# Optimization experiments

Measured on AMD Instinct MI355X. Metric: run time of the kernel, lower is better.

Reference implementation:

```python
import jax, jax.numpy as jnp
import numpy as np

HIDDEN = 4096
NUM_HEADS = 32
HEAD_DIM = HIDDEN // NUM_HEADS


def _fp8_roundtrip(x):
    # emulate torch float8_e4m3fn weight storage
    return x.astype(jnp.float8_e4m3fn).astype(jnp.float32)


def setup_inputs() -> dict:
    key = jax.random.key(0)
    ks = jax.random.split(key, 10)
    B, S = 2, 4096
    hidden_states = jax.random.normal(ks[0], (B, S, HIDDEN), dtype=jnp.float32)
    scale = 0.02
    def lin(kw, kb):
        w = jax.random.normal(kw, (HIDDEN, HIDDEN), dtype=jnp.float32) * scale
        b = jax.random.normal(kb, (HIDDEN,), dtype=jnp.float32) * scale
        return w, b
    wq, bq = lin(ks[1], ks[2])
    wk, bk = lin(ks[3], ks[4])
    wv, bv = lin(ks[5], ks[6])
    wl, bl = lin(ks[7], ks[8])
    # fp8-quantized Q/K/V projections (latent projection stays fp32)
    wq, bq = _fp8_roundtrip(wq), _fp8_roundtrip(bq)
    wk, bk = _fp8_roundtrip(wk), _fp8_roundtrip(bk)
    wv, bv = _fp8_roundtrip(wv), _fp8_roundtrip(bv)
    return {"hidden_states": hidden_states, "wq": wq, "bq": bq, "wk": wk,
            "bk": bk, "wv": wv, "bv": bv, "wl": wl, "bl": bl}


def reference(hidden_states, wq, bq, wk, bk, wv, bv, wl, bl):
    B, S, E = hidden_states.shape
    H, D = NUM_HEADS, HEAD_DIM
    q = (hidden_states @ wq.T + bq).reshape(B, S, H, D)
    k = (hidden_states @ wk.T + bk).reshape(B, S, H, D)
    v = (hidden_states @ wv.T + bv).reshape(B, S, H, D)
    latent = hidden_states @ wl.T + bl  # computed but unused, as in source
    # NOTE: source does NOT transpose to [B,H,S,D]; scores are [B,S,H,H]
    scores = jnp.einsum('bshd,bstd->bsht', q, k) / np.sqrt(D).astype(np.float32)
    probs = jax.nn.softmax(scores, axis=-1)
    context = jnp.einsum('bsht,bstd->bshd', probs, v).reshape(B, S, E)
    return context
```

## Files before the change

### kernel.cpp

```cpp
#include <hip/hip_runtime.h>
#include <stdint.h>

#define HIDDEN 4096
#define M_TOK 8192
#define KDIM 4096

typedef __attribute__((ext_vector_type(8))) __bf16 bf16x8;
typedef __attribute__((ext_vector_type(4))) float f32x4;
typedef __attribute__((ext_vector_type(8))) unsigned short u16x8;

#define GAS __attribute__((address_space(1)))
#define LAS __attribute__((address_space(3)))

__device__ __forceinline__ unsigned short f2bf(float f) {
  unsigned int u = __float_as_uint(f);
  u += 0x7FFFu + ((u >> 16) & 1u);
  return (unsigned short)(u >> 16);
}
__device__ __forceinline__ float bf2f(unsigned short b) {
  return __uint_as_float(((unsigned int)b) << 16);
}

__device__ __forceinline__ void cvt8(const float* __restrict__ in,
                                     unsigned short* __restrict__ out, int i) {
  const f32x4* p = (const f32x4*)in + (size_t)2 * i;
  f32x4 a = p[0], b = p[1];
  u16x8 o;
  o[0] = f2bf(a.x); o[1] = f2bf(a.y); o[2] = f2bf(a.z); o[3] = f2bf(a.w);
  o[4] = f2bf(b.x); o[5] = f2bf(b.y); o[6] = f2bf(b.z); o[7] = f2bf(b.w);
  ((u16x8*)out)[i] = o;
}

__global__ __launch_bounds__(256) void cvt_fused(
    const float* __restrict__ hs, const float* __restrict__ wq,
    const float* __restrict__ wk, const float* __restrict__ wv,
    const float* __restrict__ bq, const float* __restrict__ bk,
    const float* __restrict__ bv,
    unsigned short* __restrict__ hsb, unsigned short* __restrict__ wb,
    float* __restrict__ bias) {
  int b = blockIdx.x;
  int tid = threadIdx.x;
  if (b < 16384) {
    cvt8(hs, hsb, b * 256 + tid);
  } else if (b < 24576) {
    cvt8(wq, wb, (b - 16384) * 256 + tid);
  } else if (b < 32768) {
    cvt8(wk, wb + 16777216, (b - 24576) * 256 + tid);
  } else if (b < 40960) {
    cvt8(wv, wb + 33554432, (b - 32768) * 256 + tid);
  } else {
    int i = (b - 40960) * 256 + tid;
    float v = (i < 4096) ? bq[i] : (i < 8192) ? bk[i - 4096] : bv[i - 8192];
    bias[i] = v;
  }
}

#define BAR() __builtin_amdgcn_s_barrier()
#define PRIO(p) __builtin_amdgcn_s_setprio(p)
#define VMC6() asm volatile("s_waitcnt vmcnt(6)" ::: "memory")
#define VMC0() asm volatile("s_waitcnt vmcnt(0)" ::: "memory")
#define LGKM0() do { asm volatile("s_waitcnt lgkmcnt(0)" ::: "memory"); \
  __builtin_amdgcn_sched_barrier(0); } while (0)
#define SB0() __builtin_amdgcn_sched_barrier(0)

__global__ __launch_bounds__(512, 2) void gemm_qkv(
    const unsigned short* __restrict__ A,
    const unsigned short* __restrict__ W,
    const float* __restrict__ bias,
    unsigned short* __restrict__ out) {
  __shared__ __attribute__((aligned(16))) unsigned short lds[65536];

  int tid = threadIdx.x;
  int lane = tid & 63;
  int w = tid >> 6;
  int wm = w >> 2;
  int wn = w & 3;
  int l16 = lane & 15;
  int lk = lane >> 4;

  int bid = blockIdx.x;
  int xcd = bid & 7;
  int local = bid >> 3;
  int r = local >> 5;
  int i = local & 31;
  int tm = (xcd << 2) + (i >> 3);
  int tn = (r << 3) + (i & 7);
  int m0 = tm << 8, n0 = tn << 8;

  int rp = tid >> 3;
  int ce = ((tid & 7) << 3) ^ ((rp & 7) << 3);
  const unsigned short* aSrc = A + (size_t)(m0 + rp) * KDIM + ce;
  const unsigned short* bSrc = W + (size_t)(n0 + rp) * KDIM + ce;
  int tid8 = tid * 8;

#define STA(b, h, kt) do { \
  __builtin_amdgcn_global_load_lds((GAS void*)(aSrc + (size_t)((h)*128) * KDIM + (kt)*64), \
      (LAS void*)(lds + (b)*16384 + (h)*8192 + tid8), 16, 0, 0); \
  __builtin_amdgcn_global_load_lds((GAS void*)(aSrc + (size_t)((h)*128 + 64) * KDIM + (kt)*64), \
      (LAS void*)(lds + (b)*16384 + (h)*8192 + 4096 + tid8), 16, 0, 0); } while (0)
#define STB(b, h, kt) do { \
  __builtin_amdgcn_global_load_lds((GAS void*)(bSrc + (size_t)((h)*128) * KDIM + (kt)*64), \
      (LAS void*)(lds + 32768 + (b)*16384 + (h)*8192 + tid8), 16, 0, 0); \
  __builtin_amdgcn_global_load_lds((GAS void*)(bSrc + (size_t)((h)*128 + 64) * KDIM + (kt)*64), \
      (LAS void*)(lds + 32768 + (b)*16384 + (h)*8192 + 4096 + tid8), 16, 0, 0); } while (0)

  int colbase = (lk << 3) ^ ((l16 & 7) << 3);
  int aRd = wm * 8192 + l16 * 64 + colbase;
  int bRd = (wn >> 1) * 8192 + (wn & 1) * 4096 + l16 * 64 + colbase;

#define RD_A(c, mi, ks) (*(const bf16x8*)(lds + (c)*16384 + (((aRd) + (mi)*1024) ^ ((ks)*32))))
#define RD_B(c, nj, ks) (*(const bf16x8*)(lds + 32768 + (c)*16384 + (((bRd) + (nj)*1024) ^ ((ks)*32))))

  bf16x8 av[8][2];
  bf16x8 bv[4][2];
  f32x4 acc[8][4] = {};

#define RP1(c) do { \
  bv[0][0]=RD_B(c,0,0); bv[0][1]=RD_B(c,0,1); bv[1][0]=RD_B(c,1,0); bv[1][1]=RD_B(c,1,1); \
  bv[2][0]=RD_B(c,2,0); bv[2][1]=RD_B(c,2,1); bv[3][0]=RD_B(c,3,0); bv[3][1]=RD_B(c,3,1); \
  av[0][0]=RD_A(c,0,0); av[0][1]=RD_A(c,0,1); av[1][0]=RD_A(c,1,0); av[1][1]=RD_A(c,1,1); } while (0)
#define RP2(c) do { \
  av[2][0]=RD_A(c,2,0); av[2][1]=RD_A(c,2,1); av[3][0]=RD_A(c,3,0); av[3][1]=RD_A(c,3,1); \
  av[4][0]=RD_A(c,4,0); av[4][1]=RD_A(c,4,1); av[5][0]=RD_A(c,5,0); av[5][1]=RD_A(c,5,1); } while (0)
#define RP3(c) do { \
  av[6][0]=RD_A(c,6,0); av[6][1]=RD_A(c,6,1); av[7][0]=RD_A(c,7,0); av[7][1]=RD_A(c,7,1); } while (0)

#define MFMA2(mi, nj) do { \
  acc[mi][nj] = __builtin_amdgcn_mfma_f32_16x16x32_bf16(av[mi][0], bv[nj][0], acc[mi][nj], 0, 0, 0); \
  acc[mi][nj] = __builtin_amdgcn_mfma_f32_16x16x32_bf16(av[mi][1], bv[nj][1], acc[mi][nj], 0, 0, 0); } while (0)
#define MM(mi) do { MFMA2(mi,0); MFMA2(mi,1); MFMA2(mi,2); MFMA2(mi,3); } while (0)

#define KTILE(c, ka, kb) do { \
  STA(!(c), 1, ka); \
  BAR(); LGKM0(); PRIO(1); MM(0); MM(1); RP2(c); PRIO(0); SB0(); BAR(); \
  STB(c, 0, kb); \
  BAR(); LGKM0(); PRIO(1); MM(2); MM(3); RP3(c); PRIO(0); SB0(); BAR(); \
  STB(c, 1, kb); \
  BAR(); LGKM0(); PRIO(1); MM(4); MM(5); PRIO(0); SB0(); BAR(); \
  STA(c, 0, kb); VMC6(); \
  BAR(); SB0(); PRIO(1); MM(6); MM(7); RP1(!(c)); PRIO(0); SB0(); BAR(); } while (0)

  STB(0, 0, 0); STB(0, 1, 0); STA(0, 0, 0); STA(0, 1, 0);
  STB(1, 0, 1); STB(1, 1, 1); STA(1, 0, 1);
  VMC0();
  BAR();
  RP1(0);

  for (int it = 0; it < 31; ++it) {
    int k1 = 2 * it + 1, k2 = 2 * it + 2, k3 = 2 * it + 3;
    KTILE(0, k1, k2);
    KTILE(1, k2, k3);
  }
  STA(1, 1, 63);
  BAR(); LGKM0(); PRIO(1); MM(0); MM(1); RP2(0); PRIO(0); SB0(); BAR();
  BAR(); LGKM0(); PRIO(1); MM(2); MM(3); RP3(0); PRIO(0); SB0(); BAR();
  BAR(); LGKM0(); PRIO(1); MM(4); MM(5); PRIO(0); SB0(); BAR();
  VMC0();
  BAR(); SB0(); PRIO(1); MM(6); MM(7); RP1(1); PRIO(0); SB0(); BAR();
  BAR(); LGKM0(); PRIO(1); MM(0); MM(1); RP2(1); PRIO(0); SB0(); BAR();
  BAR(); LGKM0(); PRIO(1); MM(2); MM(3); RP3(1); PRIO(0); SB0(); BAR();
  BAR(); LGKM0(); PRIO(1); MM(4); MM(5); PRIO(0); SB0(); BAR();
  BAR(); LGKM0(); PRIO(1); MM(6); MM(7); PRIO(0);

  int matc = n0 >> 12;
  int ncol = (n0 & 4095) + wn * 64;
  unsigned short* O = out + (size_t)matc * M_TOK * HIDDEN;
  float bb[4];
#pragma unroll
  for (int nj = 0; nj < 4; ++nj) bb[nj] = bias[n0 + wn * 64 + nj * 16 + l16];
#pragma unroll
  for (int mi = 0; mi < 8; ++mi) {
#pragma unroll
    for (int rr = 0; rr < 4; ++rr) {
      int row = m0 + wm * 128 + mi * 16 + lk * 4 + rr;
      size_t rb = (size_t)row * HIDDEN + ncol + l16;
#pragma unroll
      for (int nj = 0; nj < 4; ++nj)
        O[rb + nj * 16] = f2bf(acc[mi][nj][rr] + bb[nj]);
    }
  }
}

__global__ __launch_bounds__(256) void attn_kernel(const unsigned short* __restrict__ qkv,
                                                   float* __restrict__ out) {
  __shared__ float sQ[32 * 132];
  __shared__ float sK[32 * 132];
  __shared__ float sV[32 * 132];
  __shared__ float sP[32 * 33];

  int m = blockIdx.x;
  int tid = threadIdx.x;
  const unsigned short* gq = qkv + (size_t)m * HIDDEN;
  const unsigned short* gk = gq + (size_t)M_TOK * HIDDEN;
  const unsigned short* gv = gk + (size_t)M_TOK * HIDDEN;

  int row = tid >> 3;
  int cb = (tid & 7) << 4;
  int go = row * 128 + cb;
  int lo = row * 132 + cb;
  {
    u16x8 x0 = *(const u16x8*)(gq + go);
    u16x8 x1 = *(const u16x8*)(gq + go + 8);
#pragma unroll
    for (int j = 0; j < 8; ++j) { sQ[lo + j] = bf2f(x0[j]); sQ[lo + 8 + j] = bf2f(x1[j]); }
    x0 = *(const u16x8*)(gk + go);
    x1 = *(const u16x8*)(gk + go + 8);
#pragma unroll
    for (int j = 0; j < 8; ++j) { sK[lo + j] = bf2f(x0[j]); sK[lo + 8 + j] = bf2f(x1[j]); }
    x0 = *(const u16x8*)(gv + go);
    x1 = *(const u16x8*)(gv + go + 8);
#pragma unroll
    for (int j = 0; j < 8; ++j) { sV[lo + j] = bf2f(x0[j]); sV[lo + 8 + j] = bf2f(x1[j]); }
  }
  __syncthreads();

  int h = tid >> 3;
  int t4 = (tid & 7) << 2;
  const f32x4* qr = (const f32x4*)(sQ + h * 132);
  const f32x4* k0 = (const f32x4*)(sK + (t4 + 0) * 132);
  const f32x4* k1 = (const f32x4*)(sK + (t4 + 1) * 132);
  const f32x4* k2 = (const f32x4*)(sK + (t4 + 2) * 132);
  const f32x4* k3 = (const f32x4*)(sK + (t4 + 3) * 132);
  float s0 = 0.f, s1 = 0.f, s2 = 0.f, s3 = 0.f;
#pragma unroll
  for (int d = 0; d < 32; ++d) {
    f32x4 q = qr[d];
    f32x4 a = k0[d]; s0 += q.x * a.x + q.y * a.y + q.z * a.z + q.w * a.w;
    f32x4 b = k1[d]; s1 += q.x * b.x + q.y * b.y + q.z * b.z + q.w * b.w;
    f32x4 c = k2[d]; s2 += q.x * c.x + q.y * c.y + q.z * c.z + q.w * c.w;
    f32x4 e = k3[d]; s3 += q.x * e.x + q.y * e.y + q.z * e.z + q.w * e.w;
  }
  const float scale = 0.08838834764831845f;
  s0 *= scale; s1 *= scale; s2 *= scale; s3 *= scale;
  float mx = fmaxf(fmaxf(s0, s1), fmaxf(s2, s3));
  mx = fmaxf(mx, __shfl_xor(mx, 1));
  mx = fmaxf(mx, __shfl_xor(mx, 2));
  mx = fmaxf(mx, __shfl_xor(mx, 4));
  float e0 = __expf(s0 - mx), e1 = __expf(s1 - mx), e2 = __expf(s2 - mx), e3 = __expf(s3 - mx);
  float sum = e0 + e1 + e2 + e3;
  sum += __shfl_xor(sum, 1);
  sum += __shfl_xor(sum, 2);
  sum += __shfl_xor(sum, 4);
  float inv = 1.0f / sum;
  sP[h * 33 + t4 + 0] = e0 * inv;
  sP[h * 33 + t4 + 1] = e1 * inv;
  sP[h * 33 + t4 + 2] = e2 * inv;
  sP[h * 33 + t4 + 3] = e3 * inv;
  __syncthreads();

  int d0 = (tid & 7) << 4;
  f32x4 o0 = {0.f, 0.f, 0.f, 0.f}, o1 = o0, o2 = o0, o3 = o0;
  const float* pr = sP + h * 33;
#pragma unroll
  for (int t = 0; t < 32; ++t) {
    float p = pr[t];
    const f32x4* vr = (const f32x4*)(sV + t * 132 + d0);
    o0 += p * vr[0];
    o1 += p * vr[1];
    o2 += p * vr[2];
    o3 += p * vr[3];
  }
  f32x4* op = (f32x4*)(out + (size_t)m * HIDDEN + h * 128 + d0);
  op[0] = o0; op[1] = o1; op[2] = o2; op[3] = o3;
}

extern "C" void kernel_launch(void* const* d_in, const int* in_sizes, int n_in,
                              void* d_out, int out_size, void* d_ws, size_t ws_size,
                              hipStream_t stream) {
  const float* hs = (const float*)d_in[0];
  const float* wq = (const float*)d_in[1];
  const float* bq = (const float*)d_in[2];
  const float* wk = (const float*)d_in[3];
  const float* bk = (const float*)d_in[4];
  const float* wv = (const float*)d_in[5];
  const float* bv = (const float*)d_in[6];

  char* ws = (char*)d_ws;
  const size_t HS_OFF = 0;
  const size_t W_OFF = 67108864;
  const size_t QKV_OFF = 167772160;
  const size_t BIAS_OFF = 369098752;
  const size_t NEED = 369147904;
  if (ws_size < NEED) return;

  unsigned short* hsb = (unsigned short*)(ws + HS_OFF);
  unsigned short* wb = (unsigned short*)(ws + W_OFF);
  unsigned short* qkv = (unsigned short*)(ws + QKV_OFF);
  float* bias = (float*)(ws + BIAS_OFF);

  cvt_fused<<<41008, 256, 0, stream>>>(hs, wq, wk, wv, bq, bk, bv, hsb, wb, bias);
  gemm_qkv<<<1536, 512, 0, stream>>>(hsb, wb, bias, qkv);
  attn_kernel<<<8192, 256, 0, stream>>>(qkv, (float*)d_out);
}
```

Baseline: 838.2 us.

## Shrink QKV GEMM tile to 128x256 with simpler K=32 double-buffered pipeline

Replaces the 256x256 tile, 512-thread GEMM with a 128x256 tile on 256 threads (4 waves each covering 128x64). K steps drop from 64 to 32 per stage, with a plain double-buffered loop that stages the next tile while computing the current one, in place of the interleaved four-phase schedule. LDS use falls from 128KB to 48KB and the grid doubles, which should raise occupancy and simplify scheduling. In exchange, arithmetic intensity per tile is lower and barriers per FLOP go up.

```diff
diff --git a/kernel.cpp b/kernel.cpp
--- a/kernel.cpp
+++ b/kernel.cpp
@@ -63,104 +63,90 @@
   __builtin_amdgcn_sched_barrier(0); } while (0)
 #define SB0() __builtin_amdgcn_sched_barrier(0)
 
-__global__ __launch_bounds__(512, 2) void gemm_qkv(
+__global__ __launch_bounds__(256, 2) void gemm_qkv(
     const unsigned short* __restrict__ A,
     const unsigned short* __restrict__ W,
     const float* __restrict__ bias,
     unsigned short* __restrict__ out) {
-  __shared__ __attribute__((aligned(16))) unsigned short lds[65536];
+  __shared__ __attribute__((aligned(16))) unsigned short lds[24576];
 
   int tid = threadIdx.x;
   int lane = tid & 63;
-  int w = tid >> 6;
-  int wm = w >> 2;
-  int wn = w & 3;
+  int wn = tid >> 6;
   int l16 = lane & 15;
   int lk = lane >> 4;
 
   int bid = blockIdx.x;
   int xcd = bid & 7;
   int local = bid >> 3;
-  int r = local >> 5;
-  int i = local & 31;
-  int tm = (xcd << 2) + (i >> 3);
+  int r = local >> 6;
+  int i = local & 63;
+  int tm = (xcd << 3) + (i >> 3);
   int tn = (r << 3) + (i & 7);
-  int m0 = tm << 8, n0 = tn << 8;
-
-  int rp = tid >> 3;
-  int ce = ((tid & 7) << 3) ^ ((rp & 7) << 3);
-  const unsigned short* aSrc = A + (size_t)(m0 + rp) * KDIM + ce;
-  const unsigned short* bSrc = W + (size_t)(n0 + rp) * KDIM + ce;
+  int m0 = tm << 7, n0 = tn << 8;
+
+  int rsub = tid >> 2;
+  int ce = (((tid & 3) ^ (rsub & 3)) << 3);
+  const unsigned short* aSrc = A + (size_t)(m0 + rsub) * KDIM + ce;
+  const unsigned short* bSrc = W + (size_t)(n0 + rsub) * KDIM + ce;
   int tid8 = tid * 8;
 
-#define STA(b, h, kt) do { \
-  __builtin_amdgcn_global_load_lds((GAS void*)(aSrc + (size_t)((h)*128) * KDIM + (kt)*64), \
-      (LAS void*)(lds + (b)*16384 + (h)*8192 + tid8), 16, 0, 0); \
-  __builtin_amdgcn_global_load_lds((GAS void*)(aSrc + (size_t)((h)*128 + 64) * KDIM + (kt)*64), \
-      (LAS void*)(lds + (b)*16384 + (h)*8192 + 4096 + tid8), 16, 0, 0); } while (0)
-#define STB(b, h, kt) do { \
-  __builtin_amdgcn_global_load_lds((GAS void*)(bSrc + (size_t)((h)*128) * KDIM + (kt)*64), \
-      (LAS void*)(lds + 32768 + (b)*16384 + (h)*8192 + tid8), 16, 0, 0); \
-  __builtin_amdgcn_global_load_lds((GAS void*)(bSrc + (size_t)((h)*128 + 64) * KDIM + (kt)*64), \
-      (LAS void*)(lds + 32768 + (b)*16384 + (h)*8192 + 4096 + tid8), 16, 0, 0); } while (0)
-
-  int colbase = (lk << 3) ^ ((l16 & 7) << 3);
-  int aRd = wm * 8192 + l16 * 64 + colbase;
-  int bRd = (wn >> 1) * 8192 + (wn & 1) * 4096 + l16 * 64 + colbase;
-
-#define RD_A(c, mi, ks) (*(const bf16x8*)(lds + (c)*16384 + (((aRd) + (mi)*1024) ^ ((ks)*32))))
-#define RD_B(c, nj, ks) (*(const bf16x8*)(lds + 32768 + (c)*16384 + (((bRd) + (nj)*1024) ^ ((ks)*32))))
-
-  bf16x8 av[8][2];
-  bf16x8 bv[4][2];
+#define STAGE(b, kt) do { \
+  __builtin_amdgcn_global_load_lds((GAS void*)(aSrc + (kt)*32), \
+      (LAS void*)(lds + (b)*4096 + tid8), 16, 0, 0); \
+  __builtin_amdgcn_global_load_lds((GAS void*)(aSrc + (size_t)64 * KDIM + (kt)*32), \
+      (LAS void*)(lds + (b)*4096 + 2048 + tid8), 16, 0, 0); \
+  __builtin_amdgcn_global_load_lds((GAS void*)(bSrc + (kt)*32), \
+      (LAS void*)(lds + 8192 + (b)*8192 + tid8), 16, 0, 0); \
+  __builtin_amdgcn_global_load_lds((GAS void*)(bSrc + (size_t)64 * KDIM + (kt)*32), \
+      (LAS void*)(lds + 8192 + (b)*8192 + 2048 + tid8), 16, 0, 0); \
+  __builtin_amdgcn_global_load_lds((GAS void*)(bSrc + (size_t)128 * KDIM + (kt)*32), \
+      (LAS void*)(lds + 8192 + (b)*8192 + 4096 + tid8), 16, 0, 0); \
+  __builtin_amdgcn_global_load_lds((GAS void*)(bSrc + (size_t)192 * KDIM + (kt)*32), \
+      (LAS void*)(lds + 8192 + (b)*8192 + 6144 + tid8), 16, 0, 0); } while (0)
+
+  int colbase = ((lk ^ (l16 & 3)) << 3);
+  int aRd = l16 * 32 + colbase;
+  int bRd = wn * 2048 + l16 * 32 + colbase;
+
+#define RD_A(c, mi) (*(const bf16x8*)(lds + (c)*4096 + aRd + (mi)*512))
+#define RD_B(c, nj) (*(const bf16x8*)(lds + 8192 + (c)*8192 + bRd + (nj)*512))
+
+  bf16x8 av[8];
+  bf16x8 bv[4];
   f32x4 acc[8][4] = {};
 
-#define RP1(c) do { \
-  bv[0][0]=RD_B(c,0,0); bv[0][1]=RD_B(c,0,1); bv[1][0]=RD_B(c,1,0); bv[1][1]=RD_B(c,1,1); \
-  bv[2][0]=RD_B(c,2,0); bv[2][1]=RD_B(c,2,1); bv[3][0]=RD_B(c,3,0); bv[3][1]=RD_B(c,3,1); \
-  av[0][0]=RD_A(c,0,0); av[0][1]=RD_A(c,0,1); av[1][0]=RD_A(c,1,0); av[1][1]=RD_A(c,1,1); } while (0)
-#define RP2(c) do { \
-  av[2][0]=RD_A(c,2,0); av[2][1]=RD_A(c,2,1); av[3][0]=RD_A(c,3,0); av[3][1]=RD_A(c,3,1); \
-  av[4][0]=RD_A(c,4,0); av[4][1]=RD_A(c,4,1); av[5][0]=RD_A(c,5,0); av[5][1]=RD_A(c,5,1); } while (0)
-#define RP3(c) do { \
-  av[6][0]=RD_A(c,6,0); av[6][1]=RD_A(c,6,1); av[7][0]=RD_A(c,7,0); av[7][1]=RD_A(c,7,1); } while (0)
-
-#define MFMA2(mi, nj) do { \
-  acc[mi][nj] = __builtin_amdgcn_mfma_f32_16x16x32_bf16(av[mi][0], bv[nj][0], acc[mi][nj], 0, 0, 0); \
-  acc[mi][nj] = __builtin_amdgcn_mfma_f32_16x16x32_bf16(av[mi][1], bv[nj][1], acc[mi][nj], 0, 0, 0); } while (0)
-#define MM(mi) do { MFMA2(mi,0); MFMA2(mi,1); MFMA2(mi,2); MFMA2(mi,3); } while (0)
-
-#define KTILE(c, ka, kb) do { \
-  STA(!(c), 1, ka); \
-  BAR(); LGKM0(); PRIO(1); MM(0); MM(1); RP2(c); PRIO(0); SB0(); BAR(); \
-  STB(c, 0, kb); \
-  BAR(); LGKM0(); PRIO(1); MM(2); MM(3); RP3(c); PRIO(0); SB0(); BAR(); \
-  STB(c, 1, kb); \
-  BAR(); LGKM0(); PRIO(1); MM(4); MM(5); PRIO(0); SB0(); BAR(); \
-  STA(c, 0, kb); VMC6(); \
-  BAR(); SB0(); PRIO(1); MM(6); MM(7); RP1(!(c)); PRIO(0); SB0(); BAR(); } while (0)
-
-  STB(0, 0, 0); STB(0, 1, 0); STA(0, 0, 0); STA(0, 1, 0);
-  STB(1, 0, 1); STB(1, 1, 1); STA(1, 0, 1);
+#define READS(c) do { \
+  bv[0] = RD_B(c,0); bv[1] = RD_B(c,1); bv[2] = RD_B(c,2); bv[3] = RD_B(c,3); \
+  av[0] = RD_A(c,0); av[1] = RD_A(c,1); av[2] = RD_A(c,2); av[3] = RD_A(c,3); \
+  av[4] = RD_A(c,4); av[5] = RD_A(c,5); av[6] = RD_A(c,6); av[7] = RD_A(c,7); } while (0)
+
+#define MF(mi, nj) acc[mi][nj] = __builtin_amdgcn_mfma_f32_16x16x32_bf16( \
+    av[mi], bv[nj], acc[mi][nj], 0, 0, 0)
+#define MROW(mi) do { MF(mi,0); MF(mi,1); MF(mi,2); MF(mi,3); } while (0)
+#define MFMAS() do { MROW(0); MROW(1); MROW(2); MROW(3); \
+                     MROW(4); MROW(5); MROW(6); MROW(7); } while (0)
+
+  STAGE(0, 0); STAGE(1, 1);
   VMC0();
   BAR();
-  RP1(0);
-
-  for (int it = 0; it < 31; ++it) {
-    int k1 = 2 * it + 1, k2 = 2 * it + 2, k3 = 2 * it + 3;
-    KTILE(0, k1, k2);
-    KTILE(1, k2, k3);
-  }
-  STA(1, 1, 63);
-  BAR(); LGKM0(); PRIO(1); MM(0); MM(1); RP2(0); PRIO(0); SB0(); BAR();
-  BAR(); LGKM0(); PRIO(1); MM(2); MM(3); RP3(0); PRIO(0); SB0(); BAR();
-  BAR(); LGKM0(); PRIO(1); MM(4); MM(5); PRIO(0); SB0(); BAR();
-  VMC0();
-  BAR(); SB0(); PRIO(1); MM(6); MM(7); RP1(1); PRIO(0); SB0(); BAR();
-  BAR(); LGKM0(); PRIO(1); MM(0); MM(1); RP2(1); PRIO(0); SB0(); BAR();
-  BAR(); LGKM0(); PRIO(1); MM(2); MM(3); RP3(1); PRIO(0); SB0(); BAR();
-  BAR(); LGKM0(); PRIO(1); MM(4); MM(5); PRIO(0); SB0(); BAR();
-  BAR(); LGKM0(); PRIO(1); MM(6); MM(7); PRIO(0);
+
+  for (int it = 0; it < 63; ++it) {
+    int kA = 2 * it + 2, kB = 2 * it + 3;
+    READS(0); LGKM0(); BAR();
+    STAGE(0, kA); SB0();
+    PRIO(1); MFMAS(); PRIO(0);
+    VMC6(); BAR();
+    READS(1); LGKM0(); BAR();
+    STAGE(1, kB); SB0();
+    PRIO(1); MFMAS(); PRIO(0);
+    VMC6(); BAR();
+  }
+  READS(0); LGKM0(); BAR();
+  PRIO(1); MFMAS(); PRIO(0);
+  VMC0(); BAR();
+  READS(1); LGKM0();
+  PRIO(1); MFMAS(); PRIO(0);
 
   int matc = n0 >> 12;
   int ncol = (n0 & 4095) + wn * 64;
@@ -172,7 +158,7 @@
   for (int mi = 0; mi < 8; ++mi) {
 #pragma unroll
     for (int rr = 0; rr < 4; ++rr) {
-      int row = m0 + wm * 128 + mi * 16 + lk * 4 + rr;
+      int row = m0 + mi * 16 + lk * 4 + rr;
       size_t rb = (size_t)row * HIDDEN + ncol + l16;
 #pragma unroll
       for (int nj = 0; nj < 4; ++nj)
@@ -289,6 +275,6 @@
   float* bias = (float*)(ws + BIAS_OFF);
 
   cvt_fused<<<41008, 256, 0, stream>>>(hs, wq, wk, wv, bq, bk, bv, hsb, wb, bias);
-  gemm_qkv<<<1536, 512, 0, stream>>>(hsb, wb, bias, qkv);
+  gemm_qkv<<<3072, 256, 0, stream>>>(hsb, wb, bias, qkv);
   attn_kernel<<<8192, 256, 0, stream>>>(qkv, (float*)d_out);
 }
```

Measured after the change: 1.098 ms. 31.0% more time.

## Rewrite per-token head attention with MFMA, one wave per token

Applied to the files above, without the earlier changes.

Replaces the scalar fp32 per-token 32x32 head attention with bf16 MFMA instructions: QK^T and PV each use 32x32x16 MFMAs. Each wave handles one token, so a block covers four tokens. Q and K are loaded straight into registers, and only V goes through LDS, transposed with an XOR swizzle. Softmax runs on the accumulator registers, and probabilities are rounded to bf16 and exchanged across half-waves to form the A operand. The aim is to cut ALU and LDS work in the attention stage, at the cost of bf16 rounding of probabilities and lane-strided fp32 output stores.

```diff
diff --git a/kernel.cpp b/kernel.cpp
--- a/kernel.cpp
+++ b/kernel.cpp
@@ -7,7 +7,9 @@
 
 typedef __attribute__((ext_vector_type(8))) __bf16 bf16x8;
 typedef __attribute__((ext_vector_type(4))) float f32x4;
+typedef __attribute__((ext_vector_type(16))) float f32x16;
 typedef __attribute__((ext_vector_type(8))) unsigned short u16x8;
+typedef __attribute__((ext_vector_type(4))) unsigned int u32x4;
 
 #define GAS __attribute__((address_space(1)))
 #define LAS __attribute__((address_space(3)))
@@ -181,87 +183,91 @@
   }
 }
 
-__global__ __launch_bounds__(256) void attn_kernel(const unsigned short* __restrict__ qkv,
-                                                   float* __restrict__ out) {
-  __shared__ float sQ[32 * 132];
-  __shared__ float sK[32 * 132];
-  __shared__ float sV[32 * 132];
-  __shared__ float sP[32 * 33];
-
-  int m = blockIdx.x;
+__global__ __launch_bounds__(256) void attn_mfma(const unsigned short* __restrict__ qkv,
+                                                 float* __restrict__ out) {
+  __shared__ unsigned short vt[4 * 4096];
+
   int tid = threadIdx.x;
+  int w = tid >> 6;
+  int lane = tid & 63;
+  int l31 = lane & 31;
+  int lg = lane >> 5;
+  int m = blockIdx.x * 4 + w;
+
   const unsigned short* gq = qkv + (size_t)m * HIDDEN;
   const unsigned short* gk = gq + (size_t)M_TOK * HIDDEN;
   const unsigned short* gv = gk + (size_t)M_TOK * HIDDEN;
-
-  int row = tid >> 3;
-  int cb = (tid & 7) << 4;
-  int go = row * 128 + cb;
-  int lo = row * 132 + cb;
+  unsigned short* vtw = vt + w * 4096;
+
+  bf16x8 kf[8], qf[8];
+#pragma unroll
+  for (int kc = 0; kc < 8; ++kc) {
+    kf[kc] = *(const bf16x8*)(gk + l31 * 128 + kc * 16 + lg * 8);
+    qf[kc] = *(const bf16x8*)(gq + l31 * 128 + kc * 16 + lg * 8);
+  }
+
   {
-    u16x8 x0 = *(const u16x8*)(gq + go);
-    u16x8 x1 = *(const u16x8*)(gq + go + 8);
-#pragma unroll
-    for (int j = 0; j < 8; ++j) { sQ[lo + j] = bf2f(x0[j]); sQ[lo + 8 + j] = bf2f(x1[j]); }
-    x0 = *(const u16x8*)(gk + go);
-    x1 = *(const u16x8*)(gk + go + 8);
-#pragma unroll
-    for (int j = 0; j < 8; ++j) { sK[lo + j] = bf2f(x0[j]); sK[lo + 8 + j] = bf2f(x1[j]); }
-    x0 = *(const u16x8*)(gv + go);
-    x1 = *(const u16x8*)(gv + go + 8);
-#pragma unroll
-    for (int j = 0; j < 8; ++j) { sV[lo + j] = bf2f(x0[j]); sV[lo + 8 + j] = bf2f(x1[j]); }
-  }
-  __syncthreads();
-
-  int h = tid >> 3;
-  int t4 = (tid & 7) << 2;
-  const f32x4* qr = (const f32x4*)(sQ + h * 132);
-  const f32x4* k0 = (const f32x4*)(sK + (t4 + 0) * 132);
-  const f32x4* k1 = (const f32x4*)(sK + (t4 + 1) * 132);
-  const f32x4* k2 = (const f32x4*)(sK + (t4 + 2) * 132);
-  const f32x4* k3 = (const f32x4*)(sK + (t4 + 3) * 132);
-  float s0 = 0.f, s1 = 0.f, s2 = 0.f, s3 = 0.f;
-#pragma unroll
-  for (int d = 0; d < 32; ++d) {
-    f32x4 q = qr[d];
-    f32x4 a = k0[d]; s0 += q.x * a.x + q.y * a.y + q.z * a.z + q.w * a.w;
-    f32x4 b = k1[d]; s1 += q.x * b.x + q.y * b.y + q.z * b.z + q.w * b.w;
-    f32x4 c = k2[d]; s2 += q.x * c.x + q.y * c.y + q.z * c.z + q.w * c.w;
-    f32x4 e = k3[d]; s3 += q.x * e.x + q.y * e.y + q.z * e.z + q.w * e.w;
-  }
+    int t = l31;
+#pragma unroll
+    for (int i = 0; i < 8; ++i) {
+      int c0 = lg * 64 + i * 8;
+      u16x8 v8 = *(const u16x8*)(gv + t * 128 + c0);
+#pragma unroll
+      for (int j = 0; j < 8; ++j) {
+        int d = c0 + j;
+        vtw[d * 32 + (((t >> 3) ^ (d & 3)) << 3) + (t & 7)] = v8[j];
+      }
+    }
+  }
+
+  f32x16 C = {};
+#pragma unroll
+  for (int kc = 0; kc < 8; ++kc)
+    C = __builtin_amdgcn_mfma_f32_32x32x16_bf16(kf[kc], qf[kc], C, 0, 0, 0);
+
   const float scale = 0.08838834764831845f;
-  s0 *= scale; s1 *= scale; s2 *= scale; s3 *= scale;
-  float mx = fmaxf(fmaxf(s0, s1), fmaxf(s2, s3));
-  mx = fmaxf(mx, __shfl_xor(mx, 1));
-  mx = fmaxf(mx, __shfl_xor(mx, 2));
-  mx = fmaxf(mx, __shfl_xor(mx, 4));
-  float e0 = __expf(s0 - mx), e1 = __expf(s1 - mx), e2 = __expf(s2 - mx), e3 = __expf(s3 - mx);
-  float sum = e0 + e1 + e2 + e3;
-  sum += __shfl_xor(sum, 1);
-  sum += __shfl_xor(sum, 2);
-  sum += __shfl_xor(sum, 4);
-  float inv = 1.0f / sum;
-  sP[h * 33 + t4 + 0] = e0 * inv;
-  sP[h * 33 + t4 + 1] = e1 * inv;
-  sP[h * 33 + t4 + 2] = e2 * inv;
-  sP[h * 33 + t4 + 3] = e3 * inv;
-  __syncthreads();
-
-  int d0 = (tid & 7) << 4;
-  f32x4 o0 = {0.f, 0.f, 0.f, 0.f}, o1 = o0, o2 = o0, o3 = o0;
-  const float* pr = sP + h * 33;
-#pragma unroll
-  for (int t = 0; t < 32; ++t) {
-    float p = pr[t];
-    const f32x4* vr = (const f32x4*)(sV + t * 132 + d0);
-    o0 += p * vr[0];
-    o1 += p * vr[1];
-    o2 += p * vr[2];
-    o3 += p * vr[3];
-  }
-  f32x4* op = (f32x4*)(out + (size_t)m * HIDDEN + h * 128 + d0);
-  op[0] = o0; op[1] = o1; op[2] = o2; op[3] = o3;
+  float p[16];
+#pragma unroll
+  for (int rr = 0; rr < 16; ++rr) p[rr] = C[rr] * scale;
+  float mx = p[0];
+#pragma unroll
+  for (int rr = 1; rr < 16; ++rr) mx = fmaxf(mx, p[rr]);
+  mx = fmaxf(mx, __shfl_xor(mx, 32));
+  float s = 0.f;
+#pragma unroll
+  for (int rr = 0; rr < 16; ++rr) { p[rr] = __expf(p[rr] - mx); s += p[rr]; }
+  s += __shfl_xor(s, 32);
+  float inv = 1.0f / s;
+#pragma unroll
+  for (int rr = 0; rr < 16; ++rr) p[rr] *= inv;
+
+  unsigned int pk[8], op[8];
+#pragma unroll
+  for (int i = 0; i < 8; ++i) {
+    pk[i] = (unsigned int)f2bf(p[2 * i]) | ((unsigned int)f2bf(p[2 * i + 1]) << 16);
+    op[i] = (unsigned int)__shfl_xor((int)pk[i], 32);
+  }
+  union { u32x4 u; bf16x8 b; } A0, A1;
+  A0.u = lg ? (u32x4){op[2], op[3], pk[2], pk[3]} : (u32x4){pk[0], pk[1], op[0], op[1]};
+  A1.u = lg ? (u32x4){op[6], op[7], pk[6], pk[7]} : (u32x4){pk[4], pk[5], op[4], op[5]};
+
+  asm volatile("s_waitcnt lgkmcnt(0)" ::: "memory");
+  __builtin_amdgcn_sched_barrier(0);
+  float* po = out + (size_t)m * HIDDEN;
+#pragma unroll
+  for (int dc = 0; dc < 4; ++dc) {
+    int row = dc * 32 + l31;
+    bf16x8 B0 = *(const bf16x8*)(vtw + row * 32 + (((0 << 1) + lg) ^ (l31 & 3)) * 8);
+    bf16x8 B1 = *(const bf16x8*)(vtw + row * 32 + (((1 << 1) + lg) ^ (l31 & 3)) * 8);
+    f32x16 D = {};
+    D = __builtin_amdgcn_mfma_f32_32x32x16_bf16(A0.b, B0, D, 0, 0, 0);
+    D = __builtin_amdgcn_mfma_f32_32x32x16_bf16(A1.b, B1, D, 0, 0, 0);
+#pragma unroll
+    for (int rr = 0; rr < 16; ++rr) {
+      int h = (rr & 3) + 8 * (rr >> 2) + 4 * lg;
+      po[h * 128 + dc * 32 + l31] = D[rr];
+    }
+  }
 }
 
 extern "C" void kernel_launch(void* const* d_in, const int* in_sizes, int n_in,
@@ -290,5 +296,5 @@
 
   cvt_fused<<<41008, 256, 0, stream>>>(hs, wq, wk, wv, bq, bk, bv, hsb, wb, bias);
   gemm_qkv<<<1536, 512, 0, stream>>>(hsb, wb, bias, qkv);
-  attn_kernel<<<8192, 256, 0, stream>>>(qkv, (float*)d_out);
-}
+  attn_mfma<<<2048, 256, 0, stream>>>(qkv, (float*)d_out);
+}
```

New measurement: 745.4 us (median of 2 runs). 1.12x faster.
